# Kernel optimization log

Measured on AMD Instinct MI355X. Metric: run time of the kernel, lower is better.

The kernel has to match this reference:

```python
import jax, jax.numpy as jnp
import numpy as np

NEG_SLOPE = 0.2

def gat_layer(x, src, dst, W, al, ar, b):
    # x: (N, F_in); W: (F_in, H*D); al/ar: (H, D); b: (H, D)
    N = x.shape[0]
    H, D = al.shape
    feat = (x @ W).reshape(N, H, D)                      # (N,H,D)
    el = jnp.sum(feat * al, axis=-1)                     # (N,H) src-side scores
    er = jnp.sum(feat * ar, axis=-1)                     # (N,H) dst-side scores
    e = jax.nn.leaky_relu(el[src] + er[dst], NEG_SLOPE)  # (E,H)
    # edge softmax over incoming edges of each dst node (numerically stable)
    m = jax.ops.segment_max(e, dst, num_segments=N)      # (N,H)
    m = jnp.where(jnp.isfinite(m), m, 0.0)               # guard isolated nodes
    ex = jnp.exp(e - m[dst])                             # (E,H)
    denom = jax.ops.segment_sum(ex, dst, num_segments=N) # (N,H)
    alpha = ex / jnp.maximum(denom[dst], 1e-30)          # (E,H)
    msg = alpha[:, :, None] * feat[src]                  # (E,H,D) gather + weight
    out = jax.ops.segment_sum(msg, dst, num_segments=N)  # (N,H,D) scatter-add
    return out + b[None]                                 # bias per head


def setup_inputs() -> dict:
    key = jax.random.key(0)
    ks = jax.random.split(key, 12)
    N, E, F_in, Dh = 100000, 1600000, 128, 64
    H1 = 2
    inp = {}
    inp['in_feat'] = jax.random.normal(ks[0], (N, F_in), dtype=jnp.float32)
    inp['src'] = jax.random.randint(ks[1], (E,), 0, N, dtype=jnp.int32)
    inp['dst'] = jax.random.randint(ks[2], (E,), 0, N, dtype=jnp.int32)
    s1 = 1.0 / np.sqrt(F_in)
    inp['W1'] = jax.random.normal(ks[3], (F_in, H1 * Dh), dtype=jnp.float32) * s1
    inp['al1'] = jax.random.normal(ks[4], (H1, Dh), dtype=jnp.float32) * 0.1
    inp['ar1'] = jax.random.normal(ks[5], (H1, Dh), dtype=jnp.float32) * 0.1
    inp['b1'] = jnp.zeros((H1, Dh), dtype=jnp.float32)
    s2 = 1.0 / np.sqrt(Dh)
    inp['W2'] = jax.random.normal(ks[6], (Dh, 1 * 2), dtype=jnp.float32) * s2
    inp['al2'] = jax.random.normal(ks[7], (1, 2), dtype=jnp.float32) * 0.1
    inp['ar2'] = jax.random.normal(ks[8], (1, 2), dtype=jnp.float32) * 0.1
    inp['b2'] = jnp.zeros((1, 2), dtype=jnp.float32)
    return inp


def reference(in_feat, src, dst, W1, al1, ar1, b1, W2, al2, ar2, b2):
    num_heads = al1.shape[0]
    h = gat_layer(in_feat, src, dst, W1, al1, ar1, b1)  # (N,2,64)
    h = jnp.sum(h, axis=1) / num_heads                  # head mean
    h = jax.nn.relu(h)
    out = gat_layer(h, src, dst, W2, al2, ar2, b2)      # (N,1,2)
    return out
```

## Files before the change

kernel.cpp:

```cpp
#include <hip/hip_runtime.h>
#include <hip/hip_bf16.h>
#include <hip/hip_fp16.h>

#define LEAKY 0.2f
#define NBMAX 1024
#define CCH   4096
#define SCAP2 3456

typedef _Float16 half8 __attribute__((ext_vector_type(8)));
typedef float f32x4 __attribute__((ext_vector_type(4)));

__device__ __forceinline__ float wave_sum64(float v) {
    #pragma unroll
    for (int m = 32; m > 0; m >>= 1) v += __shfl_xor(v, m, 64);
    return v;
}

__launch_bounds__(256)
__global__ void w1cvt_kernel(const float* __restrict__ W, __half* __restrict__ Wt) {
    int i = blockIdx.x * 256 + threadIdx.x;
    int n = i >> 7, k = i & 127;
    Wt[i] = __float2half(W[k * 128 + n]);
}

__launch_bounds__(256)
__global__ void gemm1_kernel(const float* __restrict__ X, const __half* __restrict__ Wt,
                             const float* __restrict__ al1, const float* __restrict__ ar1,
                             __half* __restrict__ feat_h,
                             float* __restrict__ el1, float* __restrict__ er1, int N) {
    __shared__ __half Al[64 * 136];
    __shared__ __half Wl[128 * 136];
    const int tid = threadIdx.x;
    const int r0 = blockIdx.x * 64;
    {
        int n = tid >> 1, h0 = (tid & 1) * 64;
        const __half* gsrc = Wt + n * 128 + h0;
        __half* ldst = Wl + n * 136 + h0;
        #pragma unroll
        for (int i = 0; i < 8; i++)
            *(uint4*)(ldst + i * 8) = *(const uint4*)(gsrc + i * 8);
    }
    {
        int r = tid >> 2, c0 = (tid & 3) * 32;
        int rr = r0 + r;
        const float* gsrc = X + (size_t)rr * 128 + c0;
        __half* ldst = Al + r * 136 + c0;
        if (rr < N) {
            #pragma unroll
            for (int i = 0; i < 8; i++) {
                float4 v = *(const float4*)(gsrc + i * 4);
                __half2 a = __floats2half2_rn(v.x, v.y);
                __half2 b = __floats2half2_rn(v.z, v.w);
                uint2 pk; pk.x = *(unsigned*)&a; pk.y = *(unsigned*)&b;
                *(uint2*)(ldst + i * 4) = pk;
            }
        } else {
            uint2 z; z.x = 0; z.y = 0;
            #pragma unroll
            for (int i = 0; i < 8; i++) *(uint2*)(ldst + i * 4) = z;
        }
    }
    __syncthreads();
    const int wv = tid >> 6, lane = tid & 63;
    const int lm = lane & 15, lq = lane >> 4;
    f32x4 acc[8];
    #pragma unroll
    for (int t = 0; t < 8; t++) acc[t] = (f32x4){0.f, 0.f, 0.f, 0.f};
    const __half* arow = Al + (wv * 16 + lm) * 136 + lq * 8;
    const __half* brow = Wl + lm * 136 + lq * 8;
    #pragma unroll
    for (int ks = 0; ks < 4; ks++) {
        half8 af = *(const half8*)(arow + ks * 32);
        #pragma unroll
        for (int nt = 0; nt < 8; nt++) {
            half8 bf = *(const half8*)(brow + nt * 16 * 136 + ks * 32);
            acc[nt] = __builtin_amdgcn_mfma_f32_16x16x32_f16(af, bf, acc[nt], 0, 0, 0);
        }
    }
    __syncthreads();
    __half* Cl = Al;
    #pragma unroll
    for (int nt = 0; nt < 8; nt++) {
        #pragma unroll
        for (int r = 0; r < 4; r++) {
            int m = wv * 16 + lq * 4 + r;
            Cl[m * 136 + nt * 16 + lm] = __float2half(acc[nt][r]);
        }
    }
    __syncthreads();
    {
        int r = tid >> 2, c0 = (tid & 3) * 32;
        int rr = r0 + r;
        float pel = 0.f, per = 0.f;
        const __half* crow = Cl + r * 136 + c0;
        if (rr < N) {
            #pragma unroll
            for (int i = 0; i < 4; i++)
                *(uint4*)(feat_h + (size_t)rr * 128 + c0 + i * 8) = *(const uint4*)(crow + i * 8);
            #pragma unroll
            for (int c = 0; c < 32; c++) {
                float fv = __half2float(crow[c]);
                pel += fv * al1[c0 + c];
                per += fv * ar1[c0 + c];
            }
        }
        pel += __shfl_xor(pel, 1, 64);
        per += __shfl_xor(per, 1, 64);
        if ((tid & 1) == 0 && rr < N) {
            int h = (tid >> 1) & 1;
            el1[rr * 2 + h] = pel;
            er1[rr * 2 + h] = per;
        }
    }
}

__launch_bounds__(256)
__global__ void bhist_kernel(const int* __restrict__ dst, int* __restrict__ bcount,
                             int E, int NB) {
    __shared__ int hls[NBMAX];
    for (int i = threadIdx.x; i < NB; i += 256) hls[i] = 0;
    __syncthreads();
    int stride = gridDim.x * 256;
    for (int e = blockIdx.x * 256 + threadIdx.x; e < E; e += stride)
        atomicAdd(&hls[dst[e] >> 7], 1);
    __syncthreads();
    for (int i = threadIdx.x; i < NB; i += 256) {
        int c = hls[i];
        if (c) atomicAdd(&bcount[i], c);
    }
}

__launch_bounds__(1024)
__global__ void bscan_kernel(const int* __restrict__ bcount, int* __restrict__ bstart,
                             int* __restrict__ bcursor, int NB) {
    __shared__ int sd[NBMAX];
    int t = threadIdx.x;
    int v = (t < NB) ? bcount[t] : 0;
    sd[t] = v;
    __syncthreads();
    for (int o = 1; o < NBMAX; o <<= 1) {
        int x = (t >= o) ? sd[t - o] : 0;
        __syncthreads();
        sd[t] += x;
        __syncthreads();
    }
    if (t < NB) { int ex = sd[t] - v; bstart[t] = ex; bcursor[t] = ex; }
}

__launch_bounds__(256)
__global__ void bscatter_kernel(const int* __restrict__ src, const int* __restrict__ dst,
                                const float* __restrict__ el1, const float* __restrict__ er1,
                                int* __restrict__ bcursor, uint2* __restrict__ erec,
                                int E, int NB) {
    __shared__ int hls[NBMAX];
    for (int i = threadIdx.x; i < NB; i += 256) hls[i] = 0;
    __syncthreads();
    const int b0 = blockIdx.x * CCH;
    uint2 ureg[16];
    int breg[16];
    #pragma unroll
    for (int k = 0; k < 16; k++) {
        int e = b0 + k * 256 + threadIdx.x;
        if (e < E) {
            int s = src[e], d = dst[e];
            int bk = d >> 7;
            breg[k] = bk;
            float2 lv = *((const float2*)el1 + s);
            float2 rv = *((const float2*)er1 + d);
            float e0 = lv.x + rv.x; e0 = (e0 > 0.f) ? e0 : LEAKY * e0;
            float e1 = lv.y + rv.y; e1 = (e1 > 0.f) ? e1 : LEAKY * e1;
            __half2 w = __floats2half2_rn(__expf(e0), __expf(e1));
            ureg[k].x = ((unsigned)s << 7) | (unsigned)(d & 127);
            ureg[k].y = *(unsigned*)&w;
            atomicAdd(&hls[bk], 1);
        } else breg[k] = -1;
    }
    __syncthreads();
    for (int b = threadIdx.x; b < NB; b += 256) {
        int c = hls[b];
        if (c) hls[b] = atomicAdd(&bcursor[b], c);
    }
    __syncthreads();
    #pragma unroll
    for (int k = 0; k < 16; k++) {
        if (breg[k] >= 0) {
            int p = atomicAdd(&hls[breg[k]], 1);
            erec[p] = ureg[k];
        }
    }
}

__launch_bounds__(256)
__global__ void bsort_kernel(const uint2* __restrict__ erec,
                             const int* __restrict__ bstart, const int* __restrict__ bcount,
                             uint2* __restrict__ erec2,
                             int* __restrict__ rowstart, int* __restrict__ plen,
                             int* __restrict__ tlen,
                             int N, int NB) {
    __shared__ uint2 sorted[SCAP2];
    __shared__ int cnt[128], prs[129], curs[128];
    const int tid = threadIdx.x;
    const int b = blockIdx.x;
    const int node0 = b << 7;
    const int nd = min(128, N - node0);
    const int ebase = bstart[b];
    int ecnt = bcount[b];
    if (ecnt > SCAP2 - 896) ecnt = SCAP2 - 896;
    const int pbase = ebase + 896 * b;
    if (tid < 128) cnt[tid] = 0;
    __syncthreads();
    for (int j = tid; j < ecnt; j += 256)
        atomicAdd(&cnt[erec[ebase + j].x & 127], 1);
    __syncthreads();
    int pv = 0;
    if (tid < 128) { pv = (cnt[tid] + 7) & ~7; curs[tid] = pv; }
    __syncthreads();
    for (int o = 1; o < 128; o <<= 1) {
        int x = 0;
        if (tid < 128 && tid >= o) x = curs[tid - o];
        __syncthreads();
        if (tid < 128) curs[tid] += x;
        __syncthreads();
    }
    if (tid < 128) prs[tid + 1] = curs[tid];
    if (tid == 0) prs[0] = 0;
    __syncthreads();
    if (tid < 128) curs[tid] = prs[tid + 1] - pv;
    __syncthreads();
    const int pecnt = prs[128];
    for (int j = tid; j < pecnt; j += 256) { sorted[j].x = 0; sorted[j].y = 0; }
    __syncthreads();
    for (int j = tid; j < ecnt; j += 256) {
        uint2 r = erec[ebase + j];
        int p = atomicAdd(&curs[r.x & 127], 1);
        uint2 o2;
        o2.x = (r.x >> 7) << 8;
        o2.y = r.y;
        sorted[p] = o2;
    }
    __syncthreads();
    for (int j = tid; j < pecnt; j += 256) erec2[(size_t)pbase + j] = sorted[j];
    if (tid < nd) {
        rowstart[node0 + tid] = pbase + prs[tid];
        plen[node0 + tid] = prs[tid + 1] - prs[tid];
        tlen[node0 + tid] = cnt[tid];
    }
}

__launch_bounds__(256)
__global__ void agg1_kernel(const char* __restrict__ fh, const uint2* __restrict__ erec2,
                            const float* __restrict__ b1, const float* __restrict__ W2,
                            const float* __restrict__ ar2,
                            const int* __restrict__ rowstart, const int* __restrict__ plen,
                            float* __restrict__ feat2, float* __restrict__ er2, int N) {
    int wid = (blockIdx.x * blockDim.x + threadIdx.x) >> 6;
    int lane = threadIdx.x & 63;
    if (wid >= N) return;
    const int len = plen[wid];
    const uint2* rp = erec2 + rowstart[wid];
    const int l5 = lane & 31;
    const int sub = lane >> 5;
    const unsigned hsh = (l5 < 16) ? 0u : 16u;
    float acc0 = 0.f, acc1 = 0.f, acc2 = 0.f, acc3 = 0.f, den = 0.f;
    for (int j = 0; j < len; j += 8) {
        uint2 r[4];
        #pragma unroll
        for (int u = 0; u < 4; u++) r[u] = rp[j + 2 * u + sub];
        uint2 v[4];
        #pragma unroll
        for (int u = 0; u < 4; u++)
            v[u] = *(const uint2*)(fh + (size_t)r[u].x + l5 * 8);
        #pragma unroll
        for (int u = 0; u < 4; u++) {
            float w = __half2float(__ushort_as_half((unsigned short)((r[u].y >> hsh) & 0xffffu)));
            den += w;
            float2 f0 = __half22float2(*(const __half2*)&v[u].x);
            float2 f1 = __half22float2(*(const __half2*)&v[u].y);
            acc0 += w * f0.x; acc1 += w * f0.y;
            acc2 += w * f1.x; acc3 += w * f1.y;
        }
    }
    acc0 += __shfl_xor(acc0, 32, 64);
    acc1 += __shfl_xor(acc1, 32, 64);
    acc2 += __shfl_xor(acc2, 32, 64);
    acc3 += __shfl_xor(acc3, 32, 64);
    den  += __shfl_xor(den,  32, 64);
    float inv = 1.f / fmaxf(den, 1e-30f);
    float4 bb = *(const float4*)(b1 + 4 * l5);
    float o0 = acc0 * inv + bb.x;
    float o1 = acc1 * inv + bb.y;
    float o2 = acc2 * inv + bb.z;
    float o3 = acc3 * inv + bb.w;
    float m0 = 0.5f * (o0 + __shfl_xor(o0, 16, 64));
    float m1 = 0.5f * (o1 + __shfl_xor(o1, 16, 64));
    float m2 = 0.5f * (o2 + __shfl_xor(o2, 16, 64));
    float m3 = 0.5f * (o3 + __shfl_xor(o3, 16, 64));
    m0 = fmaxf(m0, 0.f); m1 = fmaxf(m1, 0.f);
    m2 = fmaxf(m2, 0.f); m3 = fmaxf(m3, 0.f);
    const float* wrow = W2 + 8 * (l5 & 15);
    float4 wa = *(const float4*)wrow;
    float4 wb = *(const float4*)(wrow + 4);
    float p0 = m0 * wa.x + m1 * wa.z + m2 * wb.x + m3 * wb.z;
    float p1 = m0 * wa.y + m1 * wa.w + m2 * wb.y + m3 * wb.w;
    float c0 = 0.25f * wave_sum64(p0);
    float c1 = 0.25f * wave_sum64(p1);
    if (lane == 0) {
        float2 f2; f2.x = c0; f2.y = c1;
        *((float2*)feat2 + wid) = f2;
        er2[wid] = c0 * ar2[0] + c1 * ar2[1];
    }
}

__launch_bounds__(256)
__global__ void agg2_kernel(const float* __restrict__ feat2, const float* __restrict__ er2,
                            const float* __restrict__ al2, const float* __restrict__ b2,
                            const int* __restrict__ rowstart, const int* __restrict__ tlen,
                            const uint2* __restrict__ erec2, float* __restrict__ out, int N) {
    int node = (blockIdx.x * 256 + threadIdx.x) >> 4;
    int l4 = threadIdx.x & 15;
    if (node >= N) return;
    const int len = tlen[node];
    const uint2* rp = erec2 + rowstart[node];
    const float ern = er2[node];
    const float al20 = al2[0], al21 = al2[1];
    float den = 0.f, a0 = 0.f, a1 = 0.f;
    for (int j = l4; j < len; j += 16) {
        unsigned key = rp[j].x;
        float2 f = *((const float2*)feat2 + (key >> 8));
        float e = f.x * al20 + f.y * al21 + ern;
        e = (e > 0.f) ? e : LEAKY * e;
        float w = __expf(e);
        den += w;
        a0 += w * f.x;
        a1 += w * f.y;
    }
    #pragma unroll
    for (int m = 1; m < 16; m <<= 1) {
        den += __shfl_xor(den, m, 64);
        a0  += __shfl_xor(a0, m, 64);
        a1  += __shfl_xor(a1, m, 64);
    }
    if (l4 == 0) {
        float inv = 1.f / fmaxf(den, 1e-30f);
        float2 o;
        o.x = a0 * inv + b2[0];
        o.y = a1 * inv + b2[1];
        *((float2*)out + node) = o;
    }
}

extern "C" void kernel_launch(void* const* d_in, const int* in_sizes, int n_in,
                              void* d_out, int out_size, void* d_ws, size_t ws_size,
                              hipStream_t stream) {
    const float* in_feat = (const float*)d_in[0];
    const int*   src     = (const int*)d_in[1];
    const int*   dst     = (const int*)d_in[2];
    const float* W1      = (const float*)d_in[3];
    const float* al1     = (const float*)d_in[4];
    const float* ar1     = (const float*)d_in[5];
    const float* b1      = (const float*)d_in[6];
    const float* W2      = (const float*)d_in[7];
    const float* al2     = (const float*)d_in[8];
    const float* ar2     = (const float*)d_in[9];
    const float* b2      = (const float*)d_in[10];
    float* out = (float*)d_out;

    const int N = in_sizes[0] / 128;
    const int E = in_sizes[1];
    const int NB = (N + 127) >> 7;

    char* ws = (char*)d_ws;
    __half* feat1h = (__half*)ws;
    size_t off = (size_t)N * 128 * 2;
    float* el1 = (float*)(ws + off); off += (size_t)N * 2 * 4;
    float* er1 = (float*)(ws + off); off += (size_t)N * 2 * 4;
    float* feat2 = (float*)(ws + off); off += (size_t)N * 2 * 4;
    float* er2 = (float*)(ws + off); off += (size_t)N * 4;
    int* bcount  = (int*)(ws + off); off += NBMAX * 4;
    int* bstart  = (int*)(ws + off); off += NBMAX * 4;
    int* bcursor = (int*)(ws + off); off += NBMAX * 4;
    int* rowstart = (int*)(ws + off); off += (size_t)N * 4;
    int* plen     = (int*)(ws + off); off += (size_t)N * 4;
    int* tlen     = (int*)(ws + off); off += (size_t)N * 4;
    uint2* erec  = (uint2*)(ws + off); off += (size_t)E * 8;
    uint2* erec2 = (uint2*)(ws + off); off += ((size_t)E + 896 * NB) * 8;
    __half* W1t = (__half*)(ws + off); off += 128 * 128 * 2;
    (void)ws_size; (void)n_in; (void)out_size;

    hipMemsetAsync(bcount, 0, NBMAX * 4, stream);

    w1cvt_kernel<<<64, 256, 0, stream>>>(W1, W1t);
    gemm1_kernel<<<(N + 63) / 64, 256, 0, stream>>>(in_feat, W1t, al1, ar1,
                                                    feat1h, el1, er1, N);

    const int nblkC = (E + CCH - 1) / CCH;
    bhist_kernel<<<nblkC, 256, 0, stream>>>(dst, bcount, E, NB);
    bscan_kernel<<<1, 1024, 0, stream>>>(bcount, bstart, bcursor, NB);
    bscatter_kernel<<<nblkC, 256, 0, stream>>>(src, dst, el1, er1, bcursor, erec, E, NB);
    bsort_kernel<<<NB, 256, 0, stream>>>(erec, bstart, bcount, erec2, rowstart, plen, tlen, N, NB);

    agg1_kernel<<<(N * 64 + 255) / 256, 256, 0, stream>>>(
        (const char*)feat1h, erec2, b1, W2, ar2, rowstart, plen, feat2, er2, N);

    agg2_kernel<<<(N * 16 + 255) / 256, 256, 0, stream>>>(
        feat2, er2, al2, b2, rowstart, tlen, erec2, out, N);
}
```

Baseline: 279.8 us.

## Split edge bucket scatter into coarse and fine LDS-staged radix passes

Replaces the single-pass scatter of edge records into 782 destination buckets with a two-pass radix scheme. The first pass scatters into 64 coarse buckets of 2048 nodes each; the second refines each coarse bucket into 16 fine buckets. Both passes stage records in shared memory so that global writes come out as contiguous runs. The goal is to cut the cost of writes spread across many small, poorly coalesced segments, at the price of an extra read and write of every edge record and more workspace. The fine pass only covers NCHUNK*FCH edges per coarse bucket, which assumes a bounded, roughly uniform degree distribution.

```diff
diff --git a/kernel.cpp b/kernel.cpp
--- a/kernel.cpp
+++ b/kernel.cpp
@@ -4,7 +4,10 @@
 
 #define LEAKY 0.2f
 #define NBMAX 1024
+#define NCMAX 64
 #define CCH   4096
+#define FCH   4096
+#define NCHUNK 10
 #define SCAP2 3456
 
 typedef _Float16 half8 __attribute__((ext_vector_type(8)));
@@ -132,7 +135,7 @@
 
 __launch_bounds__(1024)
 __global__ void bscan_kernel(const int* __restrict__ bcount, int* __restrict__ bstart,
-                             int* __restrict__ bcursor, int NB) {
+                             int* __restrict__ bcursor, int* __restrict__ ccursor, int NB) {
     __shared__ int sd[NBMAX];
     int t = threadIdx.x;
     int v = (t < NB) ? bcount[t] : 0;
@@ -144,49 +147,136 @@
         sd[t] += x;
         __syncthreads();
     }
-    if (t < NB) { int ex = sd[t] - v; bstart[t] = ex; bcursor[t] = ex; }
-}
-
-__launch_bounds__(256)
-__global__ void bscatter_kernel(const int* __restrict__ src, const int* __restrict__ dst,
+    if (t < NB) {
+        int ex = sd[t] - v;
+        bstart[t] = ex; bcursor[t] = ex;
+        if ((t & 15) == 0) ccursor[t >> 4] = ex;
+    }
+}
+
+__launch_bounds__(256)
+__global__ void cscatter_kernel(const int* __restrict__ src, const int* __restrict__ dst,
                                 const float* __restrict__ el1, const float* __restrict__ er1,
-                                int* __restrict__ bcursor, uint2* __restrict__ erec,
-                                int E, int NB) {
-    __shared__ int hls[NBMAX];
-    for (int i = threadIdx.x; i < NB; i += 256) hls[i] = 0;
-    __syncthreads();
+                                int* __restrict__ ccursor, uint2* __restrict__ erec0, int E) {
+    __shared__ uint2 stage[CCH];
+    __shared__ int h[NCMAX], hs[NCMAX + 1], cur[NCMAX], gb[NCMAX];
+    const int tid = threadIdx.x;
     const int b0 = blockIdx.x * CCH;
-    uint2 ureg[16];
-    int breg[16];
+    const int tcnt = min(CCH, E - b0);
+    for (int i = tid; i < NCMAX; i += 256) h[i] = 0;
+    __syncthreads();
+    uint2 rec[16]; int cb[16];
     #pragma unroll
     for (int k = 0; k < 16; k++) {
-        int e = b0 + k * 256 + threadIdx.x;
+        int e = b0 + k * 256 + tid;
+        cb[k] = -1;
         if (e < E) {
             int s = src[e], d = dst[e];
-            int bk = d >> 7;
-            breg[k] = bk;
+            cb[k] = d >> 11;
             float2 lv = *((const float2*)el1 + s);
             float2 rv = *((const float2*)er1 + d);
             float e0 = lv.x + rv.x; e0 = (e0 > 0.f) ? e0 : LEAKY * e0;
             float e1 = lv.y + rv.y; e1 = (e1 > 0.f) ? e1 : LEAKY * e1;
             __half2 w = __floats2half2_rn(__expf(e0), __expf(e1));
-            ureg[k].x = ((unsigned)s << 7) | (unsigned)(d & 127);
-            ureg[k].y = *(unsigned*)&w;
-            atomicAdd(&hls[bk], 1);
-        } else breg[k] = -1;
-    }
-    __syncthreads();
-    for (int b = threadIdx.x; b < NB; b += 256) {
-        int c = hls[b];
-        if (c) hls[b] = atomicAdd(&bcursor[b], c);
+            rec[k].x = ((unsigned)s << 11) | (unsigned)(d & 2047);
+            rec[k].y = *(unsigned*)&w;
+            atomicAdd(&h[cb[k]], 1);
+        }
+    }
+    __syncthreads();
+    int v = (tid < NCMAX) ? h[tid] : 0;
+    if (tid < NCMAX) cur[tid] = v;
+    __syncthreads();
+    for (int o = 1; o < NCMAX; o <<= 1) {
+        int x = 0;
+        if (tid < NCMAX && tid >= o) x = cur[tid - o];
+        __syncthreads();
+        if (tid < NCMAX) cur[tid] += x;
+        __syncthreads();
+    }
+    if (tid < NCMAX) hs[tid + 1] = cur[tid];
+    if (tid == 0) hs[0] = 0;
+    __syncthreads();
+    if (tid < NCMAX) {
+        cur[tid] = hs[tid];
+        gb[tid] = (v > 0) ? atomicAdd(&ccursor[tid], v) : 0;
     }
     __syncthreads();
     #pragma unroll
     for (int k = 0; k < 16; k++) {
-        if (breg[k] >= 0) {
-            int p = atomicAdd(&hls[breg[k]], 1);
-            erec[p] = ureg[k];
-        }
+        if (cb[k] >= 0) {
+            int p = atomicAdd(&cur[cb[k]], 1);
+            stage[p] = rec[k];
+        }
+    }
+    __syncthreads();
+    for (int j = tid; j < tcnt; j += 256) {
+        int lo = 0, hi = NCMAX;
+        while (hi - lo > 1) { int mid = (lo + hi) >> 1; if (hs[mid] <= j) lo = mid; else hi = mid; }
+        erec0[(size_t)gb[lo] + (j - hs[lo])] = stage[j];
+    }
+}
+
+__launch_bounds__(256)
+__global__ void fscatter_kernel(const uint2* __restrict__ erec0, const int* __restrict__ bstart,
+                                int* __restrict__ bcursor, uint2* __restrict__ erec,
+                                int E, int NB) {
+    __shared__ uint2 stage[FCH];
+    __shared__ int h[16], hs[17], cur[16], gb[16];
+    const int c = blockIdx.x / NCHUNK;
+    const int i = blockIdx.x % NCHUNK;
+    const int cbeg = bstart[c << 4];
+    const int nf16 = (c + 1) << 4;
+    const int cend = (nf16 < NB) ? bstart[nf16] : E;
+    const int beg = cbeg + i * FCH;
+    if (beg >= cend) return;
+    const int tcnt = min(FCH, cend - beg);
+    const int tid = threadIdx.x;
+    if (tid < 16) h[tid] = 0;
+    __syncthreads();
+    uint2 rec[16]; int fb[16];
+    #pragma unroll
+    for (int k = 0; k < 16; k++) {
+        int j = k * 256 + tid;
+        fb[k] = -1;
+        if (j < tcnt) {
+            uint2 r = erec0[(size_t)beg + j];
+            rec[k] = r;
+            fb[k] = (r.x >> 7) & 15;
+            atomicAdd(&h[fb[k]], 1);
+        }
+    }
+    __syncthreads();
+    if (tid < 16) cur[tid] = h[tid];
+    __syncthreads();
+    for (int o = 1; o < 16; o <<= 1) {
+        int x = 0;
+        if (tid < 16 && tid >= o) x = cur[tid - o];
+        __syncthreads();
+        if (tid < 16) cur[tid] += x;
+        __syncthreads();
+    }
+    if (tid < 16) hs[tid + 1] = cur[tid];
+    if (tid == 0) hs[0] = 0;
+    __syncthreads();
+    if (tid < 16) {
+        cur[tid] = hs[tid];
+        int fi = (c << 4) + tid;
+        gb[tid] = (h[tid] > 0 && fi < NB) ? atomicAdd(&bcursor[fi], h[tid]) : 0;
+    }
+    __syncthreads();
+    #pragma unroll
+    for (int k = 0; k < 16; k++) {
+        if (fb[k] >= 0) {
+            int p = atomicAdd(&cur[fb[k]], 1);
+            stage[p] = rec[k];
+        }
+    }
+    __syncthreads();
+    for (int j = tid; j < tcnt; j += 256) {
+        int lo = 0, hi = 16;
+        while (hi - lo > 1) { int mid = (lo + hi) >> 1; if (hs[mid] <= j) lo = mid; else hi = mid; }
+        erec[(size_t)gb[lo] + (j - hs[lo])] = stage[j];
     }
 }
 
@@ -234,7 +324,7 @@
         uint2 r = erec[ebase + j];
         int p = atomicAdd(&curs[r.x & 127], 1);
         uint2 o2;
-        o2.x = (r.x >> 7) << 8;
+        o2.x = (r.x >> 11) << 8;
         o2.y = r.y;
         sorted[p] = o2;
     }
@@ -368,6 +458,7 @@
     const int N = in_sizes[0] / 128;
     const int E = in_sizes[1];
     const int NB = (N + 127) >> 7;
+    const int NC = (N + 2047) >> 11;
 
     char* ws = (char*)d_ws;
     __half* feat1h = (__half*)ws;
@@ -379,9 +470,11 @@
     int* bcount  = (int*)(ws + off); off += NBMAX * 4;
     int* bstart  = (int*)(ws + off); off += NBMAX * 4;
     int* bcursor = (int*)(ws + off); off += NBMAX * 4;
+    int* ccursor = (int*)(ws + off); off += NCMAX * 4;
     int* rowstart = (int*)(ws + off); off += (size_t)N * 4;
     int* plen     = (int*)(ws + off); off += (size_t)N * 4;
     int* tlen     = (int*)(ws + off); off += (size_t)N * 4;
+    uint2* erec0 = (uint2*)(ws + off); off += (size_t)E * 8;
     uint2* erec  = (uint2*)(ws + off); off += (size_t)E * 8;
     uint2* erec2 = (uint2*)(ws + off); off += ((size_t)E + 896 * NB) * 8;
     __half* W1t = (__half*)(ws + off); off += 128 * 128 * 2;
@@ -395,8 +488,9 @@
 
     const int nblkC = (E + CCH - 1) / CCH;
     bhist_kernel<<<nblkC, 256, 0, stream>>>(dst, bcount, E, NB);
-    bscan_kernel<<<1, 1024, 0, stream>>>(bcount, bstart, bcursor, NB);
-    bscatter_kernel<<<nblkC, 256, 0, stream>>>(src, dst, el1, er1, bcursor, erec, E, NB);
+    bscan_kernel<<<1, 1024, 0, stream>>>(bcount, bstart, bcursor, ccursor, NB);
+    cscatter_kernel<<<nblkC, 256, 0, stream>>>(src, dst, el1, er1, ccursor, erec0, E);
+    fscatter_kernel<<<NC * NCHUNK, 256, 0, stream>>>(erec0, bstart, bcursor, erec, E, NB);
     bsort_kernel<<<NB, 256, 0, stream>>>(erec, bstart, bcount, erec2, rowstart, plen, tlen, N, NB);
 
     agg1_kernel<<<(N * 64 + 255) / 256, 256, 0, stream>>>(
```

Result: slower. 291.9 us (+4.3%).

## Fuse dst histogram into GEMM launch, deepen agg1 unroll, use nontemporal record loads

Applied to the files above, without the earlier changes.

The destination-bucket histogram now runs as extra blocks of the GEMM kernel, reusing its shared memory. This removes one launch and lets the histogram overlap with GEMM work. The agg1 edge loop is unrolled to 16 edges per iteration, which puts more feature gathers in flight. Edge-record loads in agg1 and agg2 switch to nontemporal loads so streaming records pollute the cache less. The risks are higher register pressure in agg1 and GEMM blocks being held back behind histogram blocks.

```diff
diff --git a/kernel.cpp b/kernel.cpp
--- a/kernel.cpp
+++ b/kernel.cpp
@@ -16,6 +16,14 @@
     return v;
 }
 
+__device__ __forceinline__ uint2 nt_load_rec(const uint2* p) {
+    unsigned long long x = __builtin_nontemporal_load((const unsigned long long*)p);
+    uint2 r;
+    r.x = (unsigned)x;
+    r.y = (unsigned)(x >> 32);
+    return r;
+}
+
 __launch_bounds__(256)
 __global__ void w1cvt_kernel(const float* __restrict__ W, __half* __restrict__ Wt) {
     int i = blockIdx.x * 256 + threadIdx.x;
@@ -24,13 +32,30 @@
 }
 
 __launch_bounds__(256)
-__global__ void gemm1_kernel(const float* __restrict__ X, const __half* __restrict__ Wt,
-                             const float* __restrict__ al1, const float* __restrict__ ar1,
-                             __half* __restrict__ feat_h,
-                             float* __restrict__ el1, float* __restrict__ er1, int N) {
+__global__ void gemmhist_kernel(const float* __restrict__ X, const __half* __restrict__ Wt,
+                                const float* __restrict__ al1, const float* __restrict__ ar1,
+                                __half* __restrict__ feat_h,
+                                float* __restrict__ el1, float* __restrict__ er1, int N,
+                                const int* __restrict__ dst, int* __restrict__ bcount,
+                                int E, int NB, int gemmBlocks) {
     __shared__ __half Al[64 * 136];
     __shared__ __half Wl[128 * 136];
     const int tid = threadIdx.x;
+    if (blockIdx.x >= gemmBlocks) {
+        int* hls = (int*)Al;
+        for (int i = tid; i < NB; i += 256) hls[i] = 0;
+        __syncthreads();
+        int hb = blockIdx.x - gemmBlocks;
+        int stride = (gridDim.x - gemmBlocks) * 256;
+        for (int e = hb * 256 + tid; e < E; e += stride)
+            atomicAdd(&hls[dst[e] >> 7], 1);
+        __syncthreads();
+        for (int i = tid; i < NB; i += 256) {
+            int c = hls[i];
+            if (c) atomicAdd(&bcount[i], c);
+        }
+        return;
+    }
     const int r0 = blockIdx.x * 64;
     {
         int n = tid >> 1, h0 = (tid & 1) * 64;
@@ -114,22 +139,6 @@
     }
 }
 
-__launch_bounds__(256)
-__global__ void bhist_kernel(const int* __restrict__ dst, int* __restrict__ bcount,
-                             int E, int NB) {
-    __shared__ int hls[NBMAX];
-    for (int i = threadIdx.x; i < NB; i += 256) hls[i] = 0;
-    __syncthreads();
-    int stride = gridDim.x * 256;
-    for (int e = blockIdx.x * 256 + threadIdx.x; e < E; e += stride)
-        atomicAdd(&hls[dst[e] >> 7], 1);
-    __syncthreads();
-    for (int i = threadIdx.x; i < NB; i += 256) {
-        int c = hls[i];
-        if (c) atomicAdd(&bcount[i], c);
-    }
-}
-
 __launch_bounds__(1024)
 __global__ void bscan_kernel(const int* __restrict__ bcount, int* __restrict__ bstart,
                              int* __restrict__ bcursor, int NB) {
@@ -262,10 +271,31 @@
     const int sub = lane >> 5;
     const unsigned hsh = (l5 < 16) ? 0u : 16u;
     float acc0 = 0.f, acc1 = 0.f, acc2 = 0.f, acc3 = 0.f, den = 0.f;
-    for (int j = 0; j < len; j += 8) {
+    int j = 0;
+    for (; j + 16 <= len; j += 16) {
+        uint2 r[8];
+        #pragma unroll
+        for (int u = 0; u < 4; u++) r[u] = nt_load_rec(rp + j + 2 * u + sub);
+        #pragma unroll
+        for (int u = 0; u < 4; u++) r[4 + u] = nt_load_rec(rp + j + 8 + 2 * u + sub);
+        uint2 v[8];
+        #pragma unroll
+        for (int u = 0; u < 8; u++)
+            v[u] = *(const uint2*)(fh + (size_t)r[u].x + l5 * 8);
+        #pragma unroll
+        for (int u = 0; u < 8; u++) {
+            float w = __half2float(__ushort_as_half((unsigned short)((r[u].y >> hsh) & 0xffffu)));
+            den += w;
+            float2 f0 = __half22float2(*(const __half2*)&v[u].x);
+            float2 f1 = __half22float2(*(const __half2*)&v[u].y);
+            acc0 += w * f0.x; acc1 += w * f0.y;
+            acc2 += w * f1.x; acc3 += w * f1.y;
+        }
+    }
+    if (j < len) {
         uint2 r[4];
         #pragma unroll
-        for (int u = 0; u < 4; u++) r[u] = rp[j + 2 * u + sub];
+        for (int u = 0; u < 4; u++) r[u] = nt_load_rec(rp + j + 2 * u + sub);
         uint2 v[4];
         #pragma unroll
         for (int u = 0; u < 4; u++)
@@ -325,7 +355,8 @@
     const float al20 = al2[0], al21 = al2[1];
     float den = 0.f, a0 = 0.f, a1 = 0.f;
     for (int j = l4; j < len; j += 16) {
-        unsigned key = rp[j].x;
+        uint2 rec = nt_load_rec(rp + j);
+        unsigned key = rec.x;
         float2 f = *((const float2*)feat2 + (key >> 8));
         float e = f.x * al20 + f.y * al21 + ern;
         e = (e > 0.f) ? e : LEAKY * e;
@@ -390,11 +421,13 @@
     hipMemsetAsync(bcount, 0, NBMAX * 4, stream);
 
     w1cvt_kernel<<<64, 256, 0, stream>>>(W1, W1t);
-    gemm1_kernel<<<(N + 63) / 64, 256, 0, stream>>>(in_feat, W1t, al1, ar1,
-                                                    feat1h, el1, er1, N);
-
+
+    const int gemmBlocks = (N + 63) / 64;
     const int nblkC = (E + CCH - 1) / CCH;
-    bhist_kernel<<<nblkC, 256, 0, stream>>>(dst, bcount, E, NB);
+    gemmhist_kernel<<<gemmBlocks + nblkC, 256, 0, stream>>>(
+        in_feat, W1t, al1, ar1, feat1h, el1, er1, N,
+        dst, bcount, E, NB, gemmBlocks);
+
     bscan_kernel<<<1, 1024, 0, stream>>>(bcount, bstart, bcursor, NB);
     bscatter_kernel<<<nblkC, 256, 0, stream>>>(src, dst, el1, er1, bcursor, erec, E, NB);
     bsort_kernel<<<NB, 256, 0, stream>>>(erec, bstart, bcount, erec2, rowstart, plen, tlen, N, NB);
```

New measurement: 280.1 us. Within noise of the previous version (+0.1%).
